# Kernel tuning notes

Measured on AMD Instinct MI355X. Metric: run time of the kernel, lower is better.

## Reference

```python
import jax, jax.numpy as jnp
import numpy as np

VOCAB = 3149
T_MAX = 256
C = 128      # n_emb
H = 8        # n_heads
D = C // H   # head_size = 16
L = 6        # n blocks
FF = 4 * C
EPS = 1e-5


def _layernorm(x, g, b):
    mu = jnp.mean(x, axis=-1, keepdims=True)
    var = jnp.mean((x - mu) ** 2, axis=-1, keepdims=True)
    return (x - mu) / jnp.sqrt(var + EPS) * g + b


def setup_inputs() -> dict:
    key = jax.random.key(0)
    ks = jax.random.split(key, 24)
    s = 0.02
    inp = {
        "tokens": jax.random.randint(ks[0], (64, 256), 0, VOCAB),
        "tok_emb": jax.random.normal(ks[1], (VOCAB, C), jnp.float32) * s,
        "pos_emb": jax.random.normal(ks[2], (T_MAX, C), jnp.float32) * s,
        "Wq": jax.random.normal(ks[3], (L, H, C, D), jnp.float32) * s,
        "Wk": jax.random.normal(ks[4], (L, H, C, D), jnp.float32) * s,
        "Wv": jax.random.normal(ks[5], (L, H, C, D), jnp.float32) * s,
        "Wproj": jax.random.normal(ks[6], (L, C, C), jnp.float32) * s,
        "bproj": jnp.zeros((L, C), jnp.float32),
        "ln1_g": jnp.ones((L, C), jnp.float32),
        "ln1_b": jnp.zeros((L, C), jnp.float32),
        "ln2_g": jnp.ones((L, C), jnp.float32),
        "ln2_b": jnp.zeros((L, C), jnp.float32),
        "W1": jax.random.normal(ks[7], (L, C, FF), jnp.float32) * s,
        "b1": jnp.zeros((L, FF), jnp.float32),
        "W2": jax.random.normal(ks[8], (L, FF, C), jnp.float32) * s,
        "b2": jnp.zeros((L, C), jnp.float32),
        "lnf_g": jnp.ones((C,), jnp.float32),
        "lnf_b": jnp.zeros((C,), jnp.float32),
        "Wlm": jax.random.normal(ks[9], (C, VOCAB), jnp.float32) * s,
        "blm": jnp.zeros((VOCAB,), jnp.float32),
    }
    return inp


def reference(tokens, tok_emb, pos_emb, Wq, Wk, Wv, Wproj, bproj,
              ln1_g, ln1_b, ln2_g, ln2_b, W1, b1, W2, b2,
              lnf_g, lnf_b, Wlm, blm):
    B, T = tokens.shape
    x = tok_emb[tokens] + pos_emb[:T][None, :, :]  # (B,T,C)
    # NOTE: original code scales scores by C**-0.5 with C = n_emb (128), not head_size.
    scale = jnp.asarray(C, x.dtype) ** -0.5
    causal = jnp.tril(jnp.ones((T, T), bool))
    neg_inf = jnp.asarray(-jnp.inf, x.dtype)
    for l in range(L):
        xn = _layernorm(x, ln1_g[l], ln1_b[l])
        q = jnp.einsum('btc,hcd->bhtd', xn, Wq[l])
        k = jnp.einsum('btc,hcd->bhtd', xn, Wk[l])
        v = jnp.einsum('btc,hcd->bhtd', xn, Wv[l])
        wei = jnp.einsum('bhtd,bhsd->bhts', q, k) * scale
        wei = jnp.where(causal[None, None], wei, neg_inf)
        wei = jax.nn.softmax(wei, axis=-1)
        attn = jnp.einsum('bhts,bhsd->bhtd', wei, v)
        attn = attn.transpose(0, 2, 1, 3).reshape(B, T, C)  # concat heads
        x = x + jnp.einsum('btc,cf->btf', attn, Wproj[l]) + bproj[l]
        xn2 = _layernorm(x, ln2_g[l], ln2_b[l])
        h = jax.nn.relu(jnp.einsum('btc,cf->btf', xn2, W1[l]) + b1[l])
        x = x + jnp.einsum('btf,fc->btc', h, W2[l]) + b2[l]
    x = _layernorm(x, lnf_g, lnf_b)
    logits = jnp.einsum('btc,cv->btv', x, Wlm) + blm
    return logits
```

## Files before the change

kernel.cpp:

```cpp
#include <hip/hip_runtime.h>
#include <hip/hip_bf16.h>
#include <math.h>

#define BT   16384
#define CDIM 128
#define TSEQ 256
#define NBAT 64
#define NH   8
#define HD   16
#define NL   6
#define FFD  512
#define NV   3149

typedef __bf16 bfv8 __attribute__((ext_vector_type(8)));
typedef float  fv4  __attribute__((ext_vector_type(4)));
typedef short  s4   __attribute__((ext_vector_type(4)));
typedef unsigned short u16;
typedef unsigned int   u32;
typedef u16 u16v8 __attribute__((ext_vector_type(8)));

__device__ __forceinline__ u16 f2b(float f) {
  u32 u = __builtin_bit_cast(u32, f);
  u += 0x7FFFu + ((u >> 16) & 1u);
  return (u16)(u >> 16);
}
__device__ __forceinline__ u32 cvtpk(float lo, float hi) {
  u32 r;
  asm("v_cvt_pk_bf16_f32 %0, %1, %2" : "=v"(r) : "v"(lo), "v"(hi));
  return r;
}
__device__ __forceinline__ fv4 mfma16(s4 a, s4 b, fv4 c) {
#if __has_builtin(__builtin_amdgcn_mfma_f32_16x16x16bf16_1k)
  return __builtin_amdgcn_mfma_f32_16x16x16bf16_1k(a, b, c, 0, 0, 0);
#else
  fv4 d;
  asm volatile("v_mfma_f32_16x16x16_bf16 %0, %1, %2, %3"
               : "=v"(d) : "v"(a), "v"(b), "v"(c));
  return d;
#endif
}

__global__ __launch_bounds__(256) void embed_kernel(
    const int* __restrict__ tokens, const float* __restrict__ tok_emb,
    const float* __restrict__ pos_emb, float* __restrict__ x) {
  int i4 = blockIdx.x * 256 + threadIdx.x;
  if (i4 >= BT * CDIM / 4) return;
  int i  = i4 * 4;
  int c  = i & (CDIM - 1);
  int bt = i >> 7;
  int t  = bt & (TSEQ - 1);
  int tok = tokens[bt];
  float4 te = *(const float4*)(tok_emb + (size_t)tok * CDIM + c);
  float4 pe = *(const float4*)(pos_emb + (size_t)t * CDIM + c);
  float4 r;
  r.x = te.x + pe.x; r.y = te.y + pe.y; r.z = te.z + pe.z; r.w = te.w + pe.w;
  *(float4*)(x + i) = r;
}

__global__ __launch_bounds__(256) void packqkv_bf16(
    const float* __restrict__ Wq, const float* __restrict__ Wk,
    const float* __restrict__ Wv, u16* __restrict__ dst) {
  int idx = blockIdx.x * 256 + threadIdx.x;
  if (idx >= NL * 384 * CDIM) return;
  int c = idx & 127;
  int j = (idx >> 7) % 384;
  int l = idx / (384 * CDIM);
  int sel = j >> 7;
  int jj  = j & 127;
  int h   = jj >> 4;
  int d   = jj & 15;
  const float* W = (sel == 0) ? Wq : (sel == 1) ? Wk : Wv;
  dst[idx] = f2b(W[(((size_t)l * NH + h) * CDIM + c) * HD + d]);
}

__global__ __launch_bounds__(256) void transpose_cast_t(
    const float* __restrict__ src, u16* __restrict__ dst, int R, int C) {
  __shared__ float tile[32][33];
  int l  = blockIdx.z;
  int r0 = blockIdx.y * 32, c0 = blockIdx.x * 32;
  int tr = threadIdx.x >> 5, tc = threadIdx.x & 31;
  #pragma unroll
  for (int p = 0; p < 4; p++) {
    int r = r0 + tr + p * 8, c = c0 + tc;
    if (r < R && c < C) tile[tr + p * 8][tc] = src[((size_t)l * R + r) * C + c];
  }
  __syncthreads();
  #pragma unroll
  for (int p = 0; p < 4; p++) {
    int c = c0 + tr + p * 8, r = r0 + tc;
    if (r < R && c < C) dst[((size_t)l * C + c) * R + r] = f2b(tile[tc][tr + p * 8]);
  }
}

template<int OMODE, bool BIAS, bool RELU, int BM, int BN>
__global__ __launch_bounds__(256) void gemm_mfma(
    const u16* __restrict__ A, const u16* __restrict__ Btp,
    const float* __restrict__ bias, void* __restrict__ Cout,
    int M, int N, int K) {
  constexpr int BK = 32, PAD = 40;
  constexpr int MI = BM / 32;
  constexpr int NF = BN / 32;
  __shared__ u16 As[BM][PAD];
  __shared__ u16 Bs[BN][PAD];
  const int tid  = threadIdx.x;
  const int lane = tid & 63;
  const int wv   = tid >> 6;
  const int wm   = wv & 1;
  const int wn   = wv >> 1;
  const int m0 = blockIdx.y * BM;
  const int n0 = blockIdx.x * BN;
  const int srow = tid >> 2;
  const int sk8  = (tid & 3) * 8;
  const int fr = lane & 15;
  const int fk = (lane >> 4) * 8;

  fv4 acc[MI][NF];
  #pragma unroll
  for (int i = 0; i < MI; i++)
    #pragma unroll
    for (int j = 0; j < NF; j++) acc[i][j] = (fv4){0.f, 0.f, 0.f, 0.f};

  for (int k0 = 0; k0 < K; k0 += BK) {
    #pragma unroll
    for (int p = 0; p < BM / 64; p++) {
      int r = srow + p * 64;
      *(uint4*)&As[r][sk8] = *(const uint4*)(A + (size_t)(m0 + r) * K + k0 + sk8);
    }
    #pragma unroll
    for (int p = 0; p < BN / 64; p++) {
      int r = srow + p * 64;
      int n = n0 + r;
      uint4 v = make_uint4(0u, 0u, 0u, 0u);
      if (n < N) v = *(const uint4*)(Btp + (size_t)n * K + k0 + sk8);
      *(uint4*)&Bs[r][sk8] = v;
    }
    __syncthreads();
    bfv8 a[MI], b[NF];
    #pragma unroll
    for (int i = 0; i < MI; i++)
      a[i] = *(const bfv8*)&As[wm * (BM / 2) + i * 16 + fr][fk];
    #pragma unroll
    for (int j = 0; j < NF; j++)
      b[j] = *(const bfv8*)&Bs[wn * (BN / 2) + j * 16 + fr][fk];
    #pragma unroll
    for (int i = 0; i < MI; i++)
      #pragma unroll
      for (int j = 0; j < NF; j++)
        acc[i][j] = __builtin_amdgcn_mfma_f32_16x16x32_bf16(a[i], b[j], acc[i][j], 0, 0, 0);
    __syncthreads();
  }

  const int row0 = m0 + wm * (BM / 2);
  const int col0 = n0 + wn * (BN / 2);
  const int lr   = (lane >> 4) * 4;
  #pragma unroll
  for (int j = 0; j < NF; j++) {
    int col = col0 + j * 16 + fr;
    if (col >= N) continue;
    float bz = BIAS ? bias[col] : 0.f;
    #pragma unroll
    for (int i = 0; i < MI; i++) {
      #pragma unroll
      for (int q = 0; q < 4; q++) {
        int row = row0 + i * 16 + lr + q;
        float v = acc[i][j][q] + bz;
        if (RELU) v = fmaxf(v, 0.f);
        if (OMODE == 0)      ((u16*)Cout)[(size_t)row * N + col] = f2b(v);
        else if (OMODE == 1) ((float*)Cout)[(size_t)row * N + col] = v;
        else                 ((float*)Cout)[(size_t)row * N + col] += v;
      }
    }
  }
}

template<int OMODE, bool BIAS, bool RELU, int BM, int BN>
__global__ __launch_bounds__(256) void gemm_ln_mfma(
    const float* __restrict__ X, const u16* __restrict__ Btp,
    const float* __restrict__ lng, const float* __restrict__ lnb,
    const float* __restrict__ bias, void* __restrict__ Cout,
    int M, int N) {
  constexpr int BK = 32;
  constexpr int MI = BM / 32;
  constexpr int NF = BN / 32;
  __shared__ u16 As[BM][136];
  __shared__ u16 Bs[BN][40];
  const int tid  = threadIdx.x;
  const int lane = tid & 63;
  const int wv   = tid >> 6;
  const int wm   = wv & 1;
  const int wn   = wv >> 1;
  const int m0 = blockIdx.y * BM;
  const int n0 = blockIdx.x * BN;
  const int fr = lane & 15;
  const int fk = (lane >> 4) * 8;

  {
    const int l32  = lane & 31;
    const int rsel = lane >> 5;
    float4 gg = *(const float4*)(lng + l32 * 4);
    float4 bb = *(const float4*)(lnb + l32 * 4);
    #pragma unroll 2
    for (int it = 0; it < BM / 8; it++) {
      int r = it * 8 + wv * 2 + rsel;
      float4 v = *(const float4*)(X + (size_t)(m0 + r) * 128 + l32 * 4);
      float s = (v.x + v.y) + (v.z + v.w);
      #pragma unroll
      for (int m = 1; m < 32; m <<= 1) s += __shfl_xor(s, m);
      float mu = s * (1.f / 128.f);
      float dx = v.x - mu, dy = v.y - mu, dz = v.z - mu, dw = v.w - mu;
      float s2 = (dx * dx + dy * dy) + (dz * dz + dw * dw);
      #pragma unroll
      for (int m = 1; m < 32; m <<= 1) s2 += __shfl_xor(s2, m);
      float rstd = rsqrtf(s2 * (1.f / 128.f) + 1e-5f);
      u32 p0 = cvtpk(dx * rstd * gg.x + bb.x, dy * rstd * gg.y + bb.y);
      u32 p1 = cvtpk(dz * rstd * gg.z + bb.z, dw * rstd * gg.w + bb.w);
      *(uint2*)&As[r][l32 * 4] = make_uint2(p0, p1);
    }
  }

  fv4 acc[MI][NF];
  #pragma unroll
  for (int i = 0; i < MI; i++)
    #pragma unroll
    for (int j = 0; j < NF; j++) acc[i][j] = (fv4){0.f, 0.f, 0.f, 0.f};

  for (int k0 = 0; k0 < 128; k0 += BK) {
    #pragma unroll
    for (int p = 0; p < BN / 64; p++) {
      int ch = tid + p * 256;
      int row = ch >> 2, c8 = (ch & 3) * 8;
      int n = n0 + row;
      uint4 v = make_uint4(0u, 0u, 0u, 0u);
      if (n < N) v = *(const uint4*)(Btp + (size_t)n * 128 + k0 + c8);
      *(uint4*)&Bs[row][c8] = v;
    }
    __syncthreads();
    bfv8 a[MI], b[NF];
    #pragma unroll
    for (int i = 0; i < MI; i++)
      a[i] = *(const bfv8*)&As[wm * (BM / 2) + i * 16 + fr][k0 + fk];
    #pragma unroll
    for (int j = 0; j < NF; j++)
      b[j] = *(const bfv8*)&Bs[wn * (BN / 2) + j * 16 + fr][fk];
    #pragma unroll
    for (int i = 0; i < MI; i++)
      #pragma unroll
      for (int j = 0; j < NF; j++)
        acc[i][j] = __builtin_amdgcn_mfma_f32_16x16x32_bf16(a[i], b[j], acc[i][j], 0, 0, 0);
    __syncthreads();
  }

  const int row0 = m0 + wm * (BM / 2);
  const int col0 = n0 + wn * (BN / 2);
  const int lr   = (lane >> 4) * 4;
  #pragma unroll
  for (int j = 0; j < NF; j++) {
    int col = col0 + j * 16 + fr;
    if (col >= N) continue;
    float bz = BIAS ? bias[col] : 0.f;
    #pragma unroll
    for (int i = 0; i < MI; i++) {
      #pragma unroll
      for (int q = 0; q < 4; q++) {
        int row = row0 + i * 16 + lr + q;
        float v = acc[i][j][q] + bz;
        if (RELU) v = fmaxf(v, 0.f);
        if (OMODE == 0) ((u16*)Cout)[(size_t)row * N + col] = f2b(v);
        else            ((float*)Cout)[(size_t)row * N + col] = v;
      }
    }
  }
}

__global__ __launch_bounds__(256) void attn_mfma(
    const u16* __restrict__ qkv, u16* __restrict__ out) {
  const float scale = 0.08838834764831843f;
  __shared__ u16 Qs[128][20];
  __shared__ u16 Ks[TSEQ][20];
  __shared__ u16 Vt[HD][284];
  const int blk = blockIdx.x;
  const int qh = blk & 1;
  const int h  = (blk >> 1) & (NH - 1);
  const int b  = blk >> 4;
  const int tid = threadIdx.x;

  #pragma unroll
  for (int p = 0; p < 2; p++) {
    int idx = tid + p * 256;
    int r  = idx >> 1;
    int c8 = (idx & 1) * 8;
    const u16* base = qkv + (size_t)(b * TSEQ + r) * 384 + h * HD + c8;
    uint4 k  = *(const uint4*)(base + CDIM);
    u16v8 v  = *(const u16v8*)(base + 2 * CDIM);
    *(uint4*)&Ks[r][c8] = k;
    #pragma unroll
    for (int i = 0; i < 8; i++) Vt[c8 + i][r] = v[i];
  }
  {
    int r  = tid >> 1;
    int c8 = (tid & 1) * 8;
    const u16* base = qkv + (size_t)(b * TSEQ + qh * 128 + r) * 384 + h * HD + c8;
    *(uint4*)&Qs[r][c8] = *(const uint4*)(base);
  }
  __syncthreads();

  const int wv   = tid >> 6;
  const int lane = tid & 63;
  const int fr = lane & 15;
  const int g  = lane >> 4;

  #pragma unroll 1
  for (int qi = 0; qi < 2; qi++) {
    const int qt = qh * 8 + (qi ? (7 - wv) : wv);
    s4 qf = *(const s4*)&Qs[(qt & 7) * 16 + fr][g * 4];

    float m = -3.4e38f, l = 0.f;
    fv4 accO = (fv4){0.f, 0.f, 0.f, 0.f};

    for (int st = 0; st < qt; st++) {
      s4 kf = *(const s4*)&Ks[st * 16 + fr][g * 4];
      fv4 sc = mfma16(kf, qf, (fv4){0.f, 0.f, 0.f, 0.f});
      float s0 = sc[0] * scale, s1 = sc[1] * scale;
      float s2 = sc[2] * scale, s3 = sc[3] * scale;
      float tm = fmaxf(fmaxf(s0, s1), fmaxf(s2, s3));
      tm = fmaxf(tm, __shfl_xor(tm, 16));
      tm = fmaxf(tm, __shfl_xor(tm, 32));
      float mn = fmaxf(m, tm);
      float corr = __expf(m - mn);
      float e0 = __expf(s0 - mn), e1 = __expf(s1 - mn);
      float e2 = __expf(s2 - mn), e3 = __expf(s3 - mn);
      l = l * corr + (e0 + e1) + (e2 + e3);
      accO[0] *= corr; accO[1] *= corr; accO[2] *= corr; accO[3] *= corr;
      s4 pf = __builtin_bit_cast(s4, make_uint2(cvtpk(e0, e1), cvtpk(e2, e3)));
      s4 vf = *(const s4*)&Vt[fr][st * 16 + g * 4];
      accO = mfma16(vf, pf, accO);
      m = mn;
    }
    {
      s4 kf = *(const s4*)&Ks[qt * 16 + fr][g * 4];
      fv4 sc = mfma16(kf, qf, (fv4){0.f, 0.f, 0.f, 0.f});
      const float NEG = -3.4e38f;
      float s0 = (4 * g + 0 > fr) ? NEG : sc[0] * scale;
      float s1 = (4 * g + 1 > fr) ? NEG : sc[1] * scale;
      float s2 = (4 * g + 2 > fr) ? NEG : sc[2] * scale;
      float s3 = (4 * g + 3 > fr) ? NEG : sc[3] * scale;
      float tm = fmaxf(fmaxf(s0, s1), fmaxf(s2, s3));
      tm = fmaxf(tm, __shfl_xor(tm, 16));
      tm = fmaxf(tm, __shfl_xor(tm, 32));
      float mn = fmaxf(m, tm);
      float corr = __expf(m - mn);
      float e0 = (s0 <= -1e37f) ? 0.f : __expf(s0 - mn);
      float e1 = (s1 <= -1e37f) ? 0.f : __expf(s1 - mn);
      float e2 = (s2 <= -1e37f) ? 0.f : __expf(s2 - mn);
      float e3 = (s3 <= -1e37f) ? 0.f : __expf(s3 - mn);
      l = l * corr + (e0 + e1) + (e2 + e3);
      accO[0] *= corr; accO[1] *= corr; accO[2] *= corr; accO[3] *= corr;
      s4 pf = __builtin_bit_cast(s4, make_uint2(cvtpk(e0, e1), cvtpk(e2, e3)));
      s4 vf = *(const s4*)&Vt[fr][qt * 16 + g * 4];
      accO = mfma16(vf, pf, accO);
    }

    float lt = l;
    lt += __shfl_xor(lt, 16);
    lt += __shfl_xor(lt, 32);
    const float inv = 1.f / lt;

    const int q_glob = qt * 16 + fr;
    u32 lo = cvtpk(accO[0] * inv, accO[1] * inv);
    u32 hi = cvtpk(accO[2] * inv, accO[3] * inv);
    *(uint2*)(out + (size_t)(b * TSEQ + q_glob) * CDIM + h * HD + 4 * g) =
        make_uint2(lo, hi);
  }
}

extern "C" void kernel_launch(void* const* d_in, const int* in_sizes, int n_in,
                              void* d_out, int out_size, void* d_ws, size_t ws_size,
                              hipStream_t stream) {
  const int*   tokens  = (const int*)  d_in[0];
  const float* tok_emb = (const float*)d_in[1];
  const float* pos_emb = (const float*)d_in[2];
  const float* Wq      = (const float*)d_in[3];
  const float* Wk      = (const float*)d_in[4];
  const float* Wv      = (const float*)d_in[5];
  const float* Wproj   = (const float*)d_in[6];
  const float* bproj   = (const float*)d_in[7];
  const float* ln1_g   = (const float*)d_in[8];
  const float* ln1_b   = (const float*)d_in[9];
  const float* ln2_g   = (const float*)d_in[10];
  const float* ln2_b   = (const float*)d_in[11];
  const float* W1      = (const float*)d_in[12];
  const float* b1      = (const float*)d_in[13];
  const float* W2      = (const float*)d_in[14];
  const float* b2      = (const float*)d_in[15];
  const float* lnf_g   = (const float*)d_in[16];
  const float* lnf_b   = (const float*)d_in[17];
  const float* Wlm     = (const float*)d_in[18];
  const float* blm     = (const float*)d_in[19];
  float* out = (float*)d_out;

  char* W = (char*)d_ws;
  float* x    = (float*)(W);
  u16*   qkvb = (u16*)  (W + 12582912);
  u16*   att  = (u16*)  (W + 25165824);
  u16*   hbuf = (u16*)  (W + 29360128);
  u16*   wqkv = (u16*)  (W + 46137344);
  u16*   wpj  = (u16*)  (W + 46727168);
  u16*   w1t  = (u16*)  (W + 46923776);
  u16*   w2t  = (u16*)  (W + 47710208);
  u16*   wlmt = (u16*)  (W + 48496640);

  packqkv_bf16<<<(NL * 384 * CDIM + 255) / 256, 256, 0, stream>>>(Wq, Wk, Wv, wqkv);
  transpose_cast_t<<<dim3(4, 4, NL), 256, 0, stream>>>(Wproj, wpj, CDIM, CDIM);
  transpose_cast_t<<<dim3(16, 4, NL), 256, 0, stream>>>(W1, w1t, CDIM, FFD);
  transpose_cast_t<<<dim3(4, 16, NL), 256, 0, stream>>>(W2, w2t, FFD, CDIM);
  transpose_cast_t<<<dim3((NV + 31) / 32, 4, 1), 256, 0, stream>>>(Wlm, wlmt, CDIM, NV);
  embed_kernel<<<(BT * CDIM / 4 + 255) / 256, 256, 0, stream>>>(tokens, tok_emb, pos_emb, x);

  for (int l = 0; l < NL; l++) {
    gemm_ln_mfma<0, false, false, 64, 128><<<dim3(3, BT / 64), 256, 0, stream>>>(
        x, wqkv + (size_t)l * 384 * CDIM, ln1_g + l * CDIM, ln1_b + l * CDIM,
        nullptr, qkvb, BT, 384);
    attn_mfma<<<NBAT * NH * 2, 256, 0, stream>>>(qkvb, att);
    gemm_mfma<2, true, false, 64, 64><<<dim3(2, BT / 64), 256, 0, stream>>>(
        att, wpj + (size_t)l * CDIM * CDIM, bproj + l * CDIM, x, BT, CDIM, CDIM);
    gemm_ln_mfma<0, true, true, 64, 128><<<dim3(4, BT / 64), 256, 0, stream>>>(
        x, w1t + (size_t)l * FFD * CDIM, ln2_g + l * CDIM, ln2_b + l * CDIM,
        b1 + l * FFD, hbuf, BT, FFD);
    gemm_mfma<2, true, false, 64, 64><<<dim3(2, BT / 64), 256, 0, stream>>>(
        hbuf, w2t + (size_t)l * CDIM * FFD, b2 + l * CDIM, x, BT, CDIM, FFD);
  }
  gemm_ln_mfma<1, true, false, 128, 128><<<dim3((NV + 127) / 128, BT / 128), 256, 0, stream>>>(
      x, wlmt, lnf_g, lnf_b, blm, out, BT, NV);
}
```

Baseline: 758.3 us.

## Load GEMM tiles with direct global-to-LDS loads and whole-K staging

Replaces the register-staged GEMM kernels with a K=128 kernel that loads the entire B panel (and A, when not layer-normed) into LDS with a single barrier, using global_load_lds direct transfers into a k-chunk-major layout. The W2 GEMM gets a double-buffered variant that prefetches the next K slice through global_load_lds while the current one feeds MFMAs. The LM-head GEMM drops from 128-row to 64-row tiles. The aim is to cut per-k-step barriers and register round trips, at the cost of more LDS per block and smaller tiles for the vocab projection. Out-of-range B rows are no longer zero-filled, so the LM-head tail tile reads stale LDS, though those columns are never stored.

```diff
diff --git a/kernel.cpp b/kernel.cpp
--- a/kernel.cpp
+++ b/kernel.cpp
@@ -38,6 +38,11 @@
                : "=v"(d) : "v"(a), "v"(b), "v"(c));
   return d;
 #endif
+}
+__device__ __forceinline__ void gload16(const u16* g, u16* l) {
+  __builtin_amdgcn_global_load_lds(
+      (const __attribute__((address_space(1))) void*)g,
+      (__attribute__((address_space(3))) void*)l, 16, 0, 0);
 }
 
 __global__ __launch_bounds__(256) void embed_kernel(
@@ -92,65 +97,92 @@
   }
 }
 
-template<int OMODE, bool BIAS, bool RELU, int BM, int BN>
-__global__ __launch_bounds__(256) void gemm_mfma(
-    const u16* __restrict__ A, const u16* __restrict__ Btp,
+template<int OMODE, bool BIAS, bool RELU, bool LN_A, int BN>
+__global__ __launch_bounds__(256) void gemm_k128(
+    const void* __restrict__ Ain, const u16* __restrict__ Btp,
+    const float* __restrict__ lng, const float* __restrict__ lnb,
     const float* __restrict__ bias, void* __restrict__ Cout,
-    int M, int N, int K) {
-  constexpr int BK = 32, PAD = 40;
-  constexpr int MI = BM / 32;
+    int M, int N) {
   constexpr int NF = BN / 32;
-  __shared__ u16 As[BM][PAD];
-  __shared__ u16 Bs[BN][PAD];
+  constexpr int ASZ = LN_A ? (64 * 144) : (16 * 64 * 8);
+  __shared__ u16 AsF[ASZ];
+  __shared__ u16 BsF[16 * BN * 8];
   const int tid  = threadIdx.x;
   const int lane = tid & 63;
   const int wv   = tid >> 6;
   const int wm   = wv & 1;
   const int wn   = wv >> 1;
-  const int m0 = blockIdx.y * BM;
+  const int m0 = blockIdx.y * 64;
   const int n0 = blockIdx.x * BN;
-  const int srow = tid >> 2;
-  const int sk8  = (tid & 3) * 8;
   const int fr = lane & 15;
-  const int fk = (lane >> 4) * 8;
-
-  fv4 acc[MI][NF];
-  #pragma unroll
-  for (int i = 0; i < MI; i++)
+  const int g  = lane >> 4;
+
+  #pragma unroll
+  for (int cc = 0; cc < 4; cc++) {
+    int c = wv * 4 + cc;
+    #pragma unroll
+    for (int p = 0; p < BN / 64; p++) {
+      int n = n0 + p * 64 + lane;
+      if (n < N)
+        gload16(Btp + (size_t)n * 128 + c * 8, &BsF[(c * BN + p * 64) * 8]);
+    }
+    if (!LN_A)
+      gload16((const u16*)Ain + (size_t)(m0 + lane) * 128 + c * 8,
+              &AsF[(c * 64) * 8]);
+  }
+
+  if (LN_A) {
+    const float* X = (const float*)Ain;
+    const int l32  = lane & 31;
+    const int rsel = lane >> 5;
+    float4 gg = *(const float4*)(lng + l32 * 4);
+    float4 bb = *(const float4*)(lnb + l32 * 4);
+    #pragma unroll 2
+    for (int it = 0; it < 8; it++) {
+      int r = it * 8 + wv * 2 + rsel;
+      float4 v = *(const float4*)(X + (size_t)(m0 + r) * 128 + l32 * 4);
+      float s = (v.x + v.y) + (v.z + v.w);
+      #pragma unroll
+      for (int m = 1; m < 32; m <<= 1) s += __shfl_xor(s, m);
+      float mu = s * (1.f / 128.f);
+      float dx = v.x - mu, dy = v.y - mu, dz = v.z - mu, dw = v.w - mu;
+      float s2 = (dx * dx + dy * dy) + (dz * dz + dw * dw);
+      #pragma unroll
+      for (int m = 1; m < 32; m <<= 1) s2 += __shfl_xor(s2, m);
+      float rstd = rsqrtf(s2 * (1.f / 128.f) + 1e-5f);
+      u32 p0 = cvtpk(dx * rstd * gg.x + bb.x, dy * rstd * gg.y + bb.y);
+      u32 p1 = cvtpk(dz * rstd * gg.z + bb.z, dw * rstd * gg.w + bb.w);
+      *(uint2*)&AsF[r * 144 + l32 * 4] = make_uint2(p0, p1);
+    }
+  }
+  __syncthreads();
+
+  fv4 acc[2][NF];
+  #pragma unroll
+  for (int i = 0; i < 2; i++)
     #pragma unroll
     for (int j = 0; j < NF; j++) acc[i][j] = (fv4){0.f, 0.f, 0.f, 0.f};
 
-  for (int k0 = 0; k0 < K; k0 += BK) {
-    #pragma unroll
-    for (int p = 0; p < BM / 64; p++) {
-      int r = srow + p * 64;
-      *(uint4*)&As[r][sk8] = *(const uint4*)(A + (size_t)(m0 + r) * K + k0 + sk8);
-    }
-    #pragma unroll
-    for (int p = 0; p < BN / 64; p++) {
-      int r = srow + p * 64;
-      int n = n0 + r;
-      uint4 v = make_uint4(0u, 0u, 0u, 0u);
-      if (n < N) v = *(const uint4*)(Btp + (size_t)n * K + k0 + sk8);
-      *(uint4*)&Bs[r][sk8] = v;
-    }
-    __syncthreads();
-    bfv8 a[MI], b[NF];
-    #pragma unroll
-    for (int i = 0; i < MI; i++)
-      a[i] = *(const bfv8*)&As[wm * (BM / 2) + i * 16 + fr][fk];
+  #pragma unroll
+  for (int ks = 0; ks < 4; ks++) {
+    bfv8 a[2], b[NF];
+    #pragma unroll
+    for (int i = 0; i < 2; i++) {
+      int row = wm * 32 + i * 16 + fr;
+      if (LN_A) a[i] = *(const bfv8*)&AsF[row * 144 + ks * 32 + g * 8];
+      else      a[i] = *(const bfv8*)&AsF[((4 * ks + g) * 64 + row) * 8];
+    }
     #pragma unroll
     for (int j = 0; j < NF; j++)
-      b[j] = *(const bfv8*)&Bs[wn * (BN / 2) + j * 16 + fr][fk];
-    #pragma unroll
-    for (int i = 0; i < MI; i++)
+      b[j] = *(const bfv8*)&BsF[((4 * ks + g) * BN + wn * (BN / 2) + j * 16 + fr) * 8];
+    #pragma unroll
+    for (int i = 0; i < 2; i++)
       #pragma unroll
       for (int j = 0; j < NF; j++)
         acc[i][j] = __builtin_amdgcn_mfma_f32_16x16x32_bf16(a[i], b[j], acc[i][j], 0, 0, 0);
-    __syncthreads();
-  }
-
-  const int row0 = m0 + wm * (BM / 2);
+  }
+
+  const int row0 = m0 + wm * 32;
   const int col0 = n0 + wn * (BN / 2);
   const int lr   = (lane >> 4) * 4;
   #pragma unroll
@@ -159,7 +191,7 @@
     if (col >= N) continue;
     float bz = BIAS ? bias[col] : 0.f;
     #pragma unroll
-    for (int i = 0; i < MI; i++) {
+    for (int i = 0; i < 2; i++) {
       #pragma unroll
       for (int q = 0; q < 4; q++) {
         int row = row0 + i * 16 + lr + q;
@@ -173,100 +205,75 @@
   }
 }
 
-template<int OMODE, bool BIAS, bool RELU, int BM, int BN>
-__global__ __launch_bounds__(256) void gemm_ln_mfma(
-    const float* __restrict__ X, const u16* __restrict__ Btp,
-    const float* __restrict__ lng, const float* __restrict__ lnb,
+template<int OMODE, bool BIAS, bool RELU>
+__global__ __launch_bounds__(256) void gemm_dbuf64(
+    const u16* __restrict__ A, const u16* __restrict__ Btp,
     const float* __restrict__ bias, void* __restrict__ Cout,
-    int M, int N) {
-  constexpr int BK = 32;
-  constexpr int MI = BM / 32;
-  constexpr int NF = BN / 32;
-  __shared__ u16 As[BM][136];
-  __shared__ u16 Bs[BN][40];
+    int M, int N, int K) {
+  __shared__ u16 As[2][4][64][8];
+  __shared__ u16 Bs[2][4][64][8];
   const int tid  = threadIdx.x;
   const int lane = tid & 63;
   const int wv   = tid >> 6;
   const int wm   = wv & 1;
   const int wn   = wv >> 1;
-  const int m0 = blockIdx.y * BM;
-  const int n0 = blockIdx.x * BN;
+  const int m0 = blockIdx.y * 64;
+  const int n0 = blockIdx.x * 64;
   const int fr = lane & 15;
-  const int fk = (lane >> 4) * 8;
-
-  {
-    const int l32  = lane & 31;
-    const int rsel = lane >> 5;
-    float4 gg = *(const float4*)(lng + l32 * 4);
-    float4 bb = *(const float4*)(lnb + l32 * 4);
-    #pragma unroll 2
-    for (int it = 0; it < BM / 8; it++) {
-      int r = it * 8 + wv * 2 + rsel;
-      float4 v = *(const float4*)(X + (size_t)(m0 + r) * 128 + l32 * 4);
-      float s = (v.x + v.y) + (v.z + v.w);
-      #pragma unroll
-      for (int m = 1; m < 32; m <<= 1) s += __shfl_xor(s, m);
-      float mu = s * (1.f / 128.f);
-      float dx = v.x - mu, dy = v.y - mu, dz = v.z - mu, dw = v.w - mu;
-      float s2 = (dx * dx + dy * dy) + (dz * dz + dw * dw);
-      #pragma unroll
-      for (int m = 1; m < 32; m <<= 1) s2 += __shfl_xor(s2, m);
-      float rstd = rsqrtf(s2 * (1.f / 128.f) + 1e-5f);
-      u32 p0 = cvtpk(dx * rstd * gg.x + bb.x, dy * rstd * gg.y + bb.y);
-      u32 p1 = cvtpk(dz * rstd * gg.z + bb.z, dw * rstd * gg.w + bb.w);
-      *(uint2*)&As[r][l32 * 4] = make_uint2(p0, p1);
-    }
-  }
-
-  fv4 acc[MI][NF];
-  #pragma unroll
-  for (int i = 0; i < MI; i++)
-    #pragma unroll
-    for (int j = 0; j < NF; j++) acc[i][j] = (fv4){0.f, 0.f, 0.f, 0.f};
-
-  for (int k0 = 0; k0 < 128; k0 += BK) {
-    #pragma unroll
-    for (int p = 0; p < BN / 64; p++) {
-      int ch = tid + p * 256;
-      int row = ch >> 2, c8 = (ch & 3) * 8;
-      int n = n0 + row;
-      uint4 v = make_uint4(0u, 0u, 0u, 0u);
-      if (n < N) v = *(const uint4*)(Btp + (size_t)n * 128 + k0 + c8);
-      *(uint4*)&Bs[row][c8] = v;
-    }
-    __syncthreads();
-    bfv8 a[MI], b[NF];
-    #pragma unroll
-    for (int i = 0; i < MI; i++)
-      a[i] = *(const bfv8*)&As[wm * (BM / 2) + i * 16 + fr][k0 + fk];
-    #pragma unroll
-    for (int j = 0; j < NF; j++)
-      b[j] = *(const bfv8*)&Bs[wn * (BN / 2) + j * 16 + fr][fk];
-    #pragma unroll
-    for (int i = 0; i < MI; i++)
-      #pragma unroll
-      for (int j = 0; j < NF; j++)
+  const int g  = lane >> 4;
+
+  const u16* agA = A   + (size_t)(m0 + lane) * K + wv * 8;
+  const u16* agB = Btp + (size_t)(n0 + lane) * K + wv * 8;
+
+  gload16(agA, &As[0][wv][0][0]);
+  gload16(agB, &Bs[0][wv][0][0]);
+
+  fv4 acc[2][2];
+  #pragma unroll
+  for (int i = 0; i < 2; i++)
+    #pragma unroll
+    for (int j = 0; j < 2; j++) acc[i][j] = (fv4){0.f, 0.f, 0.f, 0.f};
+
+  __syncthreads();
+  int cur = 0;
+  for (int k0 = 0; k0 < K; k0 += 32) {
+    if (k0 + 32 < K) {
+      gload16(agA + k0 + 32, &As[cur ^ 1][wv][0][0]);
+      gload16(agB + k0 + 32, &Bs[cur ^ 1][wv][0][0]);
+    }
+    bfv8 a[2], b[2];
+    #pragma unroll
+    for (int i = 0; i < 2; i++)
+      a[i] = *(const bfv8*)&As[cur][g][wm * 32 + i * 16 + fr][0];
+    #pragma unroll
+    for (int j = 0; j < 2; j++)
+      b[j] = *(const bfv8*)&Bs[cur][g][wn * 32 + j * 16 + fr][0];
+    #pragma unroll
+    for (int i = 0; i < 2; i++)
+      #pragma unroll
+      for (int j = 0; j < 2; j++)
         acc[i][j] = __builtin_amdgcn_mfma_f32_16x16x32_bf16(a[i], b[j], acc[i][j], 0, 0, 0);
     __syncthreads();
-  }
-
-  const int row0 = m0 + wm * (BM / 2);
-  const int col0 = n0 + wn * (BN / 2);
+    cur ^= 1;
+  }
+
+  const int row0 = m0 + wm * 32;
+  const int col0 = n0 + wn * 32;
   const int lr   = (lane >> 4) * 4;
   #pragma unroll
-  for (int j = 0; j < NF; j++) {
+  for (int j = 0; j < 2; j++) {
     int col = col0 + j * 16 + fr;
-    if (col >= N) continue;
     float bz = BIAS ? bias[col] : 0.f;
     #pragma unroll
-    for (int i = 0; i < MI; i++) {
+    for (int i = 0; i < 2; i++) {
       #pragma unroll
       for (int q = 0; q < 4; q++) {
         int row = row0 + i * 16 + lr + q;
         float v = acc[i][j][q] + bz;
         if (RELU) v = fmaxf(v, 0.f);
-        if (OMODE == 0) ((u16*)Cout)[(size_t)row * N + col] = f2b(v);
-        else            ((float*)Cout)[(size_t)row * N + col] = v;
+        if (OMODE == 0)      ((u16*)Cout)[(size_t)row * N + col] = f2b(v);
+        else if (OMODE == 1) ((float*)Cout)[(size_t)row * N + col] = v;
+        else                 ((float*)Cout)[(size_t)row * N + col] += v;
       }
     }
   }
@@ -417,18 +424,19 @@
   embed_kernel<<<(BT * CDIM / 4 + 255) / 256, 256, 0, stream>>>(tokens, tok_emb, pos_emb, x);
 
   for (int l = 0; l < NL; l++) {
-    gemm_ln_mfma<0, false, false, 64, 128><<<dim3(3, BT / 64), 256, 0, stream>>>(
+    gemm_k128<0, false, false, true, 128><<<dim3(3, BT / 64), 256, 0, stream>>>(
         x, wqkv + (size_t)l * 384 * CDIM, ln1_g + l * CDIM, ln1_b + l * CDIM,
         nullptr, qkvb, BT, 384);
     attn_mfma<<<NBAT * NH * 2, 256, 0, stream>>>(qkvb, att);
-    gemm_mfma<2, true, false, 64, 64><<<dim3(2, BT / 64), 256, 0, stream>>>(
-        att, wpj + (size_t)l * CDIM * CDIM, bproj + l * CDIM, x, BT, CDIM, CDIM);
-    gemm_ln_mfma<0, true, true, 64, 128><<<dim3(4, BT / 64), 256, 0, stream>>>(
+    gemm_k128<2, true, false, false, 64><<<dim3(2, BT / 64), 256, 0, stream>>>(
+        att, wpj + (size_t)l * CDIM * CDIM, nullptr, nullptr,
+        bproj + l * CDIM, x, BT, CDIM);
+    gemm_k128<0, true, true, true, 128><<<dim3(4, BT / 64), 256, 0, stream>>>(
         x, w1t + (size_t)l * FFD * CDIM, ln2_g + l * CDIM, ln2_b + l * CDIM,
         b1 + l * FFD, hbuf, BT, FFD);
-    gemm_mfma<2, true, false, 64, 64><<<dim3(2, BT / 64), 256, 0, stream>>>(
+    gemm_dbuf64<2, true, false><<<dim3(2, BT / 64), 256, 0, stream>>>(
         hbuf, w2t + (size_t)l * CDIM * FFD, b2 + l * CDIM, x, BT, CDIM, FFD);
   }
-  gemm_ln_mfma<1, true, false, 128, 128><<<dim3((NV + 127) / 128, BT / 128), 256, 0, stream>>>(
+  gemm_k128<1, true, false, true, 128><<<dim3((NV + 127) / 128, BT / 64), 256, 0, stream>>>(
       x, wlmt, lnf_g, lnf_b, blm, out, BT, NV);
 }
```

Result: no change. 763.4 us (+0.7%).
